# Kernel tuning notes

Measured on AMD Instinct MI355X. Metric: run time of the kernel, lower is better.

Reference implementation:

```python
import jax, jax.numpy as jnp
import numpy as np
from jax import lax

# PointPWC multi-scale Chamfer/Smoothness/Curvature loss (single scale here).
F_CHAMFER = 1.0
F_SMOOTH = 0.5
F_CURVATURE = 0.3
ALPHA0 = 0.02


def _sqdist(src, dst):
    # src: (B,N,3), dst: (B,M,3) -> (B,N,M) squared euclidean distances
    d = -2.0 * jnp.einsum('bnc,bmc->bnm', src, dst)
    d = d + jnp.sum(src * src, axis=-1)[:, :, None]
    d = d + jnp.sum(dst * dst, axis=-1)[:, None, :]
    return d


def _knn(sqd, k):
    # smallest-k of sqd along last axis -> (dists, indices)
    neg, idx = lax.top_k(-sqd, k)
    return -neg, idx


def _group(points, idx):
    # points: (B,N,C), idx: (B,M,k) -> (B,M,k,C)
    return jax.vmap(lambda p, i: p[i])(points, idx)


def _curvature(pc):
    # pc: (B,N,3) -> (B,N,3)
    _, kidx = _knn(_sqdist(pc, pc), 10)
    grouped = _group(pc, kidx)
    return jnp.sum(grouped - pc[:, :, None, :], axis=2) / 9.0


def _curvature_warp(pc, warped):
    _, kidx = _knn(_sqdist(pc, pc), 10)
    grouped = _group(warped, kidx)
    return jnp.sum(grouped - warped[:, :, None, :], axis=2) / 9.0


def _chamfer(p1, p2):
    sqd = _sqdist(p1, p2)
    return jnp.min(sqd, axis=-1), jnp.min(sqd, axis=1)


def _smooth(pc, flow, k):
    _, kidx = _knn(_sqdist(pc, pc), k)
    g = _group(flow, kidx)
    d = g - flow[:, :, None, :]
    sq = jnp.sum(d * d, axis=3)
    # safe norm: zero (self-neighbor) entries get norm 0 with zero grad
    nrm = jnp.where(sq == 0, 0.0, jnp.sqrt(jnp.where(sq == 0, 1.0, sq)))
    return jnp.sum(nrm, axis=2) / 8.0


def _interp_curvature(p1, p2, c2):
    dist, kidx = _knn(_sqdist(p1, p2), 5)
    g = _group(c2, kidx)  # (B,N,5,3)
    w = 1.0 / (dist + 1e-8)
    w = w / jnp.sum(w, axis=2, keepdims=True)
    return jnp.sum(w[..., None] * g, axis=2)


def setup_inputs() -> dict:
    key = jax.random.key(0)
    k1, k2, k3 = jax.random.split(key, 3)
    N = 8192
    coords = jax.random.normal(k1, (N, 3), dtype=jnp.float32)
    registration_gt = jax.random.normal(k2, (1, N, 3), dtype=jnp.float32)
    registration_pred = jax.random.normal(k3, (1, N, 3), dtype=jnp.float32)
    return {
        'registration_pred': registration_pred,
        'registration_gt': registration_gt,
        'coords': coords,
        'smoothness_k': 9,
    }


def reference(registration_pred, registration_gt, coords, smoothness_k):
    pc1 = coords[None]                       # (1,N,3)
    pc2 = coords[None] + registration_gt     # (1,N,3)
    flow = registration_pred                 # (1,N,3)

    pc2_curv = _curvature(pc2)
    pc1_warp = pc1 + flow
    dist1, dist2 = _chamfer(pc1_warp, pc2)
    moved_curv = _curvature_warp(pc1, pc1_warp)

    chamfer = jnp.mean(jnp.sum(dist1, axis=1)) + jnp.mean(jnp.sum(dist2, axis=1))
    smooth = jnp.mean(jnp.sum(_smooth(pc1, flow, smoothness_k), axis=1))
    inter_curv = _interp_curvature(pc1_warp, pc2, pc2_curv)
    curv = jnp.mean(jnp.sum(jnp.sum((inter_curv - moved_curv) ** 2, axis=2), axis=1))

    total = (F_CHAMFER * ALPHA0 * chamfer
             + F_CURVATURE * ALPHA0 * curv
             + F_SMOOTH * ALPHA0 * smooth)
    return jnp.reshape(total, (1,))
```

## Files before the change

kernel.cpp:

```cpp
#include <hip/hip_runtime.h>
#include <math.h>

#define N_PTS 8192
#define QPW 4
#define QPW_REV 8
#define WPB 4
#define QPB (QPW * WPB)
#define BLKS_TOPK (N_PTS / QPB)
#define BLKS_REV  (N_PTS / (QPW_REV * WPB))

#define R0_END BLKS_TOPK
#define R1_END (2 * BLKS_TOPK)
#define R3_END (3 * BLKS_TOPK)
#define GRID_TOTAL (3 * BLKS_TOPK + BLKS_REV)

#define W_CHAM 0.02f
#define W_CURV 0.006f
#define W_SMOO 0.01f

#define BIGF 1e30f
#define IDX_MASK 0x1FFFu
#define KEY_MASK 0xFFFFE000u

__device__ __forceinline__ float mkkey(float d, unsigned idx) {
    return __uint_as_float((__float_as_uint(d) & KEY_MASK) | idx);
}
__device__ __forceinline__ int keyidx(float k) {
    return (int)(__float_as_uint(k) & IDX_MASK);
}
__device__ __forceinline__ unsigned monou(float k) {
    int b = __float_as_int(k);
    return (unsigned)(b ^ ((b >> 31) | 0x80000000));
}
__device__ __forceinline__ int prefcnt(unsigned long long m) {
    return __builtin_amdgcn_mbcnt_hi((unsigned)(m >> 32),
           __builtin_amdgcn_mbcnt_lo((unsigned)m, 0));
}

template <int K>
__device__ __forceinline__ void kinsert(float kv, float (&bd)[K]) {
    bd[K - 1] = kv;
#pragma unroll
    for (int s = K - 1; s > 0; --s) {
        float lo = fminf(bd[s - 1], bd[s]);
        float hi = fmaxf(bd[s - 1], bd[s]);
        bd[s - 1] = lo; bd[s] = hi;
    }
}

template <int K>
__device__ void merge_keys(float m1, float m2, float m3, float (&bd)[K], int lane) {
    float h0 = m1, h1 = m2, h2 = m3;
#pragma unroll
    for (int r = 0; r < K; ++r) {
        float bv = h0;
#pragma unroll
        for (int off = 1; off < 64; off <<= 1) bv = fminf(bv, __shfl_xor(bv, off));
        bd[r] = bv;
        if (h0 == bv) { h0 = h1; h1 = h2; h2 = BIGF; }
    }
}

template <int K>
__device__ void tau_rescan(const float4* __restrict__ cand,
                           float nqx, float nqy, float nqz, float tau,
                           float (&bd)[K], int lane) {
#pragma unroll
    for (int r = 0; r < K; ++r) bd[r] = BIGF;
    const float4* cp = cand + lane;
    unsigned ib = (unsigned)lane;
    for (int it = 0; it < N_PTS / 64; ++it) {
        float4 p = cp[it * 64];
        float d = fmaf(p.x, nqx, fmaf(p.y, nqy, fmaf(p.z, nqz, p.w)));
        float kc = mkkey(d, ib);
        unsigned long long m = __ballot(kc <= tau);
        while (m) {
            int b = __builtin_ctzll(m);
            m &= m - 1;
            float kv = __shfl(kc, b);
            if (kv < bd[K - 1]) kinsert<K>(kv, bd);
        }
        ib += 64;
    }
}

template <int K>
__device__ void select_set(const float4* __restrict__ cand,
                           float nqx, float nqy, float nqz,
                           float& k1, float& k2, float& k3,
                           bool& q1, bool& q2, bool& q3, float& km, int lane) {
    const unsigned u1 = monou(k1), u2 = monou(k2), u3 = monou(k3);
    float bmn = k1, bmx = k1;
#pragma unroll
    for (int off = 1; off < 64; off <<= 1) {
        bmn = fminf(bmn, __shfl_xor(bmn, off));
        bmx = fmaxf(bmx, __shfl_xor(bmx, off));
    }
    unsigned lo = monou(bmn), hi = monou(bmx), piv = 0u;
    int cnt = -1;
    unsigned long long b3 = 0ull;
    for (int it = 0; it < 34; ++it) {
        piv = lo + ((hi - lo) >> 1);
        unsigned long long b1 = __ballot(u1 <= piv);
        unsigned long long b2 = __ballot(u2 <= piv);
        b3 = __ballot(u3 <= piv);
        cnt = __popcll(b1) + __popcll(b2) + __popcll(b3);
        if (cnt == K) break;
        if (cnt < K) lo = piv + 1; else hi = piv - 1;
    }
    bool setok = (cnt == K);
    bool fail;
    float bdK[K];
    if (setok) {
        q1 = (u1 <= piv); q2 = (u2 <= piv); q3 = (u3 <= piv);
        float t = q3 ? k3 : (q2 ? k2 : (q1 ? k1 : -BIGF));
#pragma unroll
        for (int off = 1; off < 64; off <<= 1) t = fmaxf(t, __shfl_xor(t, off));
        km = t;
        fail = (b3 != 0ull);
    } else {
        merge_keys<K>(k1, k2, k3, bdK, lane);
        km = bdK[K - 1];
        fail = (__ballot(k3 <= km) != 0ull);
    }
    if (fail) { tau_rescan<K>(cand, nqx, nqy, nqz, km, bdK, lane); setok = false; }
    if (!setok) {
        float kv = BIGF;
#pragma unroll
        for (int r = 0; r < K; ++r) if (lane == r) kv = bdK[r];
        k1 = kv; k2 = BIGF; k3 = BIGF;
        q1 = (lane < K); q2 = false; q3 = false;
        km = bdK[K - 1];
    }
}

__device__ __forceinline__ void wave_add3(float& a, float& b, float& c) {
#pragma unroll
    for (int off = 1; off < 64; off <<= 1) {
        a += __shfl_xor(a, off);
        b += __shfl_xor(b, off);
        c += __shfl_xor(c, off);
    }
}
__device__ __forceinline__ void wave_add4(float& a, float& b, float& c, float& d) {
#pragma unroll
    for (int off = 1; off < 64; off <<= 1) {
        a += __shfl_xor(a, off);
        b += __shfl_xor(b, off);
        c += __shfl_xor(c, off);
        d += __shfl_xor(d, off);
    }
}

template <int Q>
__device__ __forceinline__ void scank(const float4* __restrict__ cand,
                                      const float (&nqx)[Q], const float (&nqy)[Q],
                                      const float (&nqz)[Q],
                                      float (&m1)[Q], float (&m2)[Q], float (&m3)[Q],
                                      int lane) {
#pragma unroll
    for (int qi = 0; qi < Q; ++qi) { m1[qi] = BIGF; m2[qi] = BIGF; m3[qi] = BIGF; }
    const float4* cp = cand + lane;
    unsigned ib = (unsigned)lane;
#pragma unroll 2
    for (int it = 0; it < N_PTS / 256; ++it) {
        float4 p0 = cp[it * 256 + 0];
        float4 p1 = cp[it * 256 + 64];
        float4 p2 = cp[it * 256 + 128];
        float4 p3 = cp[it * 256 + 192];
#pragma unroll
        for (int qi = 0; qi < Q; ++qi) {
            float d0 = fmaf(p0.x, nqx[qi], fmaf(p0.y, nqy[qi], fmaf(p0.z, nqz[qi], p0.w)));
            float k0 = mkkey(d0, ib);
            m3[qi] = __builtin_amdgcn_fmed3f(k0, m2[qi], m3[qi]);
            m2[qi] = __builtin_amdgcn_fmed3f(k0, m1[qi], m2[qi]);
            m1[qi] = fminf(k0, m1[qi]);
            float d1 = fmaf(p1.x, nqx[qi], fmaf(p1.y, nqy[qi], fmaf(p1.z, nqz[qi], p1.w)));
            float k1 = mkkey(d1, ib + 64u);
            m3[qi] = __builtin_amdgcn_fmed3f(k1, m2[qi], m3[qi]);
            m2[qi] = __builtin_amdgcn_fmed3f(k1, m1[qi], m2[qi]);
            m1[qi] = fminf(k1, m1[qi]);
            float d2 = fmaf(p2.x, nqx[qi], fmaf(p2.y, nqy[qi], fmaf(p2.z, nqz[qi], p2.w)));
            float k2 = mkkey(d2, ib + 128u);
            m3[qi] = __builtin_amdgcn_fmed3f(k2, m2[qi], m3[qi]);
            m2[qi] = __builtin_amdgcn_fmed3f(k2, m1[qi], m2[qi]);
            m1[qi] = fminf(k2, m1[qi]);
            float d3 = fmaf(p3.x, nqx[qi], fmaf(p3.y, nqy[qi], fmaf(p3.z, nqz[qi], p3.w)));
            float k3 = mkkey(d3, ib + 192u);
            m3[qi] = __builtin_amdgcn_fmed3f(k3, m2[qi], m3[qi]);
            m2[qi] = __builtin_amdgcn_fmed3f(k3, m1[qi], m2[qi]);
            m1[qi] = fminf(k3, m1[qi]);
        }
        ib += 256u;
    }
}

__global__ void prep_kernel(const float* __restrict__ flow, const float* __restrict__ gt,
                            const float* __restrict__ coords,
                            float4* __restrict__ p1q, float4* __restrict__ p2q,
                            float4* __restrict__ wq, float* __restrict__ accs,
                            int* __restrict__ done) {
    int i = blockIdx.x * blockDim.x + threadIdx.x;
    if (i < N_PTS) {
        float cx = coords[3 * i + 0], cy = coords[3 * i + 1], cz = coords[3 * i + 2];
        float p2x = cx + gt[3 * i + 0], p2y = cy + gt[3 * i + 1], p2z = cz + gt[3 * i + 2];
        float wx = cx + flow[3 * i + 0], wy = cy + flow[3 * i + 1], wz = cz + flow[3 * i + 2];
        p1q[i] = make_float4(cx, cy, cz, cx * cx + cy * cy + cz * cz);
        p2q[i] = make_float4(p2x, p2y, p2z, p2x * p2x + p2y * p2y + p2z * p2z);
        wq[i]  = make_float4(wx, wy, wz, wx * wx + wy * wy + wz * wz);
    }
    if (i < 8) accs[i] = 0.0f;
    if (i == 8) done[0] = 0;
}

__global__ __launch_bounds__(256) void fused4_kernel(const float4* __restrict__ p1q,
                                                     const float4* __restrict__ p2q,
                                                     const float4* __restrict__ wq,
                                                     const float* __restrict__ flow,
                                                     const int* __restrict__ ksm_p,
                                                     float* __restrict__ curv2,
                                                     float* __restrict__ mcurv,
                                                     float* __restrict__ crossk,
                                                     float* __restrict__ accs) {
    const int tid = threadIdx.x, lane = tid & 63, wv = tid >> 6;
    const int b = blockIdx.x;

    if (b >= R3_END) {
        __shared__ float pmn[WPB];
        const int q0 = (b - R3_END) * (QPW_REV * WPB) + wv * QPW_REV;
        float nqx[QPW_REV], nqy[QPW_REV], nqz[QPW_REV], qw[QPW_REV], mn[QPW_REV];
#pragma unroll
        for (int qi = 0; qi < QPW_REV; ++qi) {
            float4 t = p2q[q0 + qi];
            nqx[qi] = -2.f * t.x; nqy[qi] = -2.f * t.y; nqz[qi] = -2.f * t.z;
            qw[qi] = t.w; mn[qi] = BIGF;
        }
        const float4* cp = wq + lane;
#pragma unroll 2
        for (int it = 0; it < N_PTS / 128; ++it) {
            float4 p0 = cp[it * 128 + 0];
            float4 p1 = cp[it * 128 + 64];
#pragma unroll
            for (int qi = 0; qi < QPW_REV; ++qi) {
                float d0 = fmaf(p0.x, nqx[qi], fmaf(p0.y, nqy[qi], fmaf(p0.z, nqz[qi], p0.w)));
                float d1 = fmaf(p1.x, nqx[qi], fmaf(p1.y, nqy[qi], fmaf(p1.z, nqz[qi], p1.w)));
                mn[qi] = fminf(mn[qi], fminf(d0, d1));
            }
        }
        float s = 0.f;
#pragma unroll
        for (int qi = 0; qi < QPW_REV; ++qi) {
            float v = mn[qi];
#pragma unroll
            for (int off = 1; off < 64; off <<= 1) v = fminf(v, __shfl_xor(v, off));
            s += v + qw[qi];
        }
        if (lane == 0) pmn[wv] = s;
        __syncthreads();
        if (tid == 0) atomicAdd(&accs[1], pmn[0] + pmn[1] + pmn[2] + pmn[3]);
        return;
    }

    const int role = (b < R0_END) ? 0 : (b < R1_END) ? 1 : 3;
    const int blk = b - ((role == 0) ? 0 : (role == 1) ? R0_END : R1_END);
    const int q0 = blk * QPB + wv * QPW;

    const float4* qsrc = (role == 0) ? p2q : (role == 1) ? p1q : wq;
    const float4* cand = (role == 1) ? p1q : p2q;
    float nqx[QPW], nqy[QPW], nqz[QPW];
#pragma unroll
    for (int qi = 0; qi < QPW; ++qi) {
        float4 t = qsrc[q0 + qi];
        nqx[qi] = -2.f * t.x; nqy[qi] = -2.f * t.y; nqz[qi] = -2.f * t.z;
    }
    float m1[QPW], m2[QPW], m3[QPW];
    scank<QPW>(cand, nqx, nqy, nqz, m1, m2, m3, lane);

    if (role == 3) {
        constexpr int K = 5;
#pragma unroll
        for (int qi = 0; qi < QPW; ++qi) {
            float k1 = m1[qi], k2 = m2[qi], k3 = m3[qi]; bool q1, q2, q3; float km;
            select_set<K>(p2q, nqx[qi], nqy[qi], nqz[qi], k1, k2, k3, q1, q2, q3, km, lane);
            const int q = q0 + qi;
            unsigned long long b1 = __ballot(q1), b2 = __ballot(q2), b3 = __ballot(q3);
            int c1 = __popcll(b1), c2 = __popcll(b2);
            if (q1) crossk[prefcnt(b1) * N_PTS + q] = k1;
            if (q2) crossk[(c1 + prefcnt(b2)) * N_PTS + q] = k2;
            if (q3) crossk[(c1 + c2 + prefcnt(b3)) * N_PTS + q] = k3;
        }
        return;
    }

    constexpr int K = 10;
    if (role == 0) {
#pragma unroll
        for (int qi = 0; qi < QPW; ++qi) {
            float k1 = m1[qi], k2 = m2[qi], k3 = m3[qi]; bool q1, q2, q3; float km;
            select_set<K>(p2q, nqx[qi], nqy[qi], nqz[qi], k1, k2, k3, q1, q2, q3, km, lane);
            float ax = 0.f, ay = 0.f, az = 0.f;
            if (q1) { float4 nb = p2q[keyidx(k1)]; ax += nb.x; ay += nb.y; az += nb.z; }
            if (q2) { float4 nb = p2q[keyidx(k2)]; ax += nb.x; ay += nb.y; az += nb.z; }
            if (q3) { float4 nb = p2q[keyidx(k3)]; ax += nb.x; ay += nb.y; az += nb.z; }
            wave_add3(ax, ay, az);
            if (lane == 0) {
                const int q = q0 + qi;
                float4 t = p2q[q];
                curv2[q * 3 + 0] = (ax - 10.f * t.x) * (1.f / 9.f);
                curv2[q * 3 + 1] = (ay - 10.f * t.y) * (1.f / 9.f);
                curv2[q * 3 + 2] = (az - 10.f * t.z) * (1.f / 9.f);
            }
        }
    } else {
        __shared__ float psm[WPB];
        const bool iall = (ksm_p[0] >= 10);
        float smsum = 0.f;
#pragma unroll
        for (int qi = 0; qi < QPW; ++qi) {
            float k1 = m1[qi], k2 = m2[qi], k3 = m3[qi]; bool q1, q2, q3; float km;
            select_set<K>(p1q, nqx[qi], nqy[qi], nqz[qi], k1, k2, k3, q1, q2, q3, km, lane);
            const int q = q0 + qi;
            const float fqx = flow[q * 3 + 0], fqy = flow[q * 3 + 1], fqz = flow[q * 3 + 2];
            float ax = 0.f, ay = 0.f, az = 0.f, sm = 0.f;
            if (q1) {
                const int ni = keyidx(k1);
                float4 nb = wq[ni];
                ax += nb.x; ay += nb.y; az += nb.z;
                if (iall || k1 < km) {
                    float dx = flow[ni * 3 + 0] - fqx, dy = flow[ni * 3 + 1] - fqy, dz = flow[ni * 3 + 2] - fqz;
                    float sq = dx * dx + dy * dy + dz * dz;
                    sm += (sq == 0.f) ? 0.f : sqrtf(sq);
                }
            }
            if (q2) {
                const int ni = keyidx(k2);
                float4 nb = wq[ni];
                ax += nb.x; ay += nb.y; az += nb.z;
                if (iall || k2 < km) {
                    float dx = flow[ni * 3 + 0] - fqx, dy = flow[ni * 3 + 1] - fqy, dz = flow[ni * 3 + 2] - fqz;
                    float sq = dx * dx + dy * dy + dz * dz;
                    sm += (sq == 0.f) ? 0.f : sqrtf(sq);
                }
            }
            if (q3) {
                const int ni = keyidx(k3);
                float4 nb = wq[ni];
                ax += nb.x; ay += nb.y; az += nb.z;
                if (iall || k3 < km) {
                    float dx = flow[ni * 3 + 0] - fqx, dy = flow[ni * 3 + 1] - fqy, dz = flow[ni * 3 + 2] - fqz;
                    float sq = dx * dx + dy * dy + dz * dz;
                    sm += (sq == 0.f) ? 0.f : sqrtf(sq);
                }
            }
            wave_add4(ax, ay, az, sm);
            smsum += sm * 0.125f;
            if (lane == 0) {
                float4 wqp = wq[q];
                mcurv[q * 3 + 0] = (ax - 10.f * wqp.x) * (1.f / 9.f);
                mcurv[q * 3 + 1] = (ay - 10.f * wqp.y) * (1.f / 9.f);
                mcurv[q * 3 + 2] = (az - 10.f * wqp.z) * (1.f / 9.f);
            }
        }
        if (lane == 0) psm[wv] = smsum;
        __syncthreads();
        if (tid == 0) atomicAdd(&accs[2], psm[0] + psm[1] + psm[2] + psm[3]);
    }
}

__global__ __launch_bounds__(64) void epi_kernel(const float* __restrict__ crossk,
                                                 const float4* __restrict__ wq,
                                                 const float4* __restrict__ p2q,
                                                 const float* __restrict__ curv2,
                                                 const float* __restrict__ mcurv,
                                                 float* __restrict__ accs,
                                                 int* __restrict__ done,
                                                 float* __restrict__ out) {
    const int lane = threadIdx.x & 63;
    const int q = blockIdx.x * 64 + threadIdx.x;
    constexpr int K = 5;
    float4 qp = wq[q];
    float bd[K]; int bi[K];
#pragma unroll
    for (int r = 0; r < K; ++r) {
        bi[r] = keyidx(crossk[r * N_PTS + q]);
        float4 nb = p2q[bi[r]];
        float dx = qp.x - nb.x, dy = qp.y - nb.y, dz = qp.z - nb.z;
        bd[r] = dx * dx + dy * dy + dz * dz;
    }
    float w[K], wsum = 0.f;
#pragma unroll
    for (int r = 0; r < K; ++r) { w[r] = 1.f / (bd[r] + 1e-8f); wsum += w[r]; }
    float ix = 0.f, iy = 0.f, iz = 0.f;
#pragma unroll
    for (int r = 0; r < K; ++r) {
        float ww = w[r] / wsum;
        ix += ww * curv2[bi[r] * 3 + 0];
        iy += ww * curv2[bi[r] * 3 + 1];
        iz += ww * curv2[bi[r] * 3 + 2];
    }
    float dx = ix - mcurv[q * 3 + 0];
    float dy = iy - mcurv[q * 3 + 1];
    float dz = iz - mcurv[q * 3 + 2];
    float d1 = fminf(fminf(fminf(bd[0], bd[1]), fminf(bd[2], bd[3])), bd[4]);
    float cv = dx * dx + dy * dy + dz * dz;
#pragma unroll
    for (int off = 1; off < 64; off <<= 1) {
        d1 += __shfl_xor(d1, off);
        cv += __shfl_xor(cv, off);
    }
    if (lane == 0) {
        atomicAdd(&accs[0], d1);
        atomicAdd(&accs[3], cv);
        __threadfence();
        int v = atomicAdd(done, 1);
        if (v == (int)gridDim.x - 1) {
            out[0] = W_CHAM * (accs[0] + accs[1]) + W_CURV * accs[3] + W_SMOO * accs[2];
        }
    }
}

extern "C" void kernel_launch(void* const* d_in, const int* in_sizes, int n_in,
                              void* d_out, int out_size, void* d_ws, size_t ws_size,
                              hipStream_t stream) {
    const float* flow   = (const float*)d_in[0];
    const float* gt     = (const float*)d_in[1];
    const float* coords = (const float*)d_in[2];
    const int*   ksm    = (const int*)d_in[3];

    float4* p1q   = (float4*)d_ws;
    float4* p2q   = p1q + N_PTS;
    float4* wq    = p2q + N_PTS;
    float*  curv2 = (float*)(wq + N_PTS);
    float*  mcurv = curv2 + 3 * N_PTS;
    float*  crossk = mcurv + 3 * N_PTS;
    float*  accs  = crossk + 5 * N_PTS;
    int*    done  = (int*)(accs + 8);
    float*  out   = (float*)d_out;

    prep_kernel<<<(N_PTS + 255) / 256, 256, 0, stream>>>(flow, gt, coords, p1q, p2q, wq,
                                                         accs, done);
    fused4_kernel<<<GRID_TOTAL, 256, 0, stream>>>(p1q, p2q, wq, flow, ksm,
                                                  curv2, mcurv, crossk, accs);
    epi_kernel<<<N_PTS / 64, 64, 0, stream>>>(crossk, wq, p2q, curv2, mcurv,
                                              accs, done, out);
}
```

Measured before the change: 144.9 us.

## Stage candidate points through double-buffered LDS tiles in brute-force scans

The candidate scans in both the top-k and reverse-chamfer paths now cooperatively load 512-point strips into a double-buffered shared-memory tile instead of each wave reading candidates straight from global memory. The four waves in a block share each strip, which cuts redundant global/L2 traffic. In exchange it adds a block-wide barrier per strip and 16 KB of LDS per block, which can lower occupancy. The per-point math is unchanged.

```diff
diff --git a/kernel.cpp b/kernel.cpp
--- a/kernel.cpp
+++ b/kernel.cpp
@@ -13,6 +13,9 @@
 #define R1_END (2 * BLKS_TOPK)
 #define R3_END (3 * BLKS_TOPK)
 #define GRID_TOTAL (3 * BLKS_TOPK + BLKS_REV)
+
+#define STRIP 512
+#define NSTRIP (N_PTS / STRIP)
 
 #define W_CHAM 0.02f
 #define W_CURV 0.006f
@@ -153,45 +156,57 @@
 }
 
 template <int Q>
-__device__ __forceinline__ void scank(const float4* __restrict__ cand,
-                                      const float (&nqx)[Q], const float (&nqy)[Q],
-                                      const float (&nqz)[Q],
-                                      float (&m1)[Q], float (&m2)[Q], float (&m3)[Q],
-                                      int lane) {
+__device__ __forceinline__ void scank_lds(const float4* __restrict__ cand,
+                                          float4 (&tile)[2][STRIP],
+                                          const float (&nqx)[Q], const float (&nqy)[Q],
+                                          const float (&nqz)[Q],
+                                          float (&m1)[Q], float (&m2)[Q], float (&m3)[Q],
+                                          int tid, int lane) {
 #pragma unroll
     for (int qi = 0; qi < Q; ++qi) { m1[qi] = BIGF; m2[qi] = BIGF; m3[qi] = BIGF; }
-    const float4* cp = cand + lane;
-    unsigned ib = (unsigned)lane;
-#pragma unroll 2
-    for (int it = 0; it < N_PTS / 256; ++it) {
-        float4 p0 = cp[it * 256 + 0];
-        float4 p1 = cp[it * 256 + 64];
-        float4 p2 = cp[it * 256 + 128];
-        float4 p3 = cp[it * 256 + 192];
-#pragma unroll
-        for (int qi = 0; qi < Q; ++qi) {
-            float d0 = fmaf(p0.x, nqx[qi], fmaf(p0.y, nqy[qi], fmaf(p0.z, nqz[qi], p0.w)));
-            float k0 = mkkey(d0, ib);
-            m3[qi] = __builtin_amdgcn_fmed3f(k0, m2[qi], m3[qi]);
-            m2[qi] = __builtin_amdgcn_fmed3f(k0, m1[qi], m2[qi]);
-            m1[qi] = fminf(k0, m1[qi]);
-            float d1 = fmaf(p1.x, nqx[qi], fmaf(p1.y, nqy[qi], fmaf(p1.z, nqz[qi], p1.w)));
-            float k1 = mkkey(d1, ib + 64u);
-            m3[qi] = __builtin_amdgcn_fmed3f(k1, m2[qi], m3[qi]);
-            m2[qi] = __builtin_amdgcn_fmed3f(k1, m1[qi], m2[qi]);
-            m1[qi] = fminf(k1, m1[qi]);
-            float d2 = fmaf(p2.x, nqx[qi], fmaf(p2.y, nqy[qi], fmaf(p2.z, nqz[qi], p2.w)));
-            float k2 = mkkey(d2, ib + 128u);
-            m3[qi] = __builtin_amdgcn_fmed3f(k2, m2[qi], m3[qi]);
-            m2[qi] = __builtin_amdgcn_fmed3f(k2, m1[qi], m2[qi]);
-            m1[qi] = fminf(k2, m1[qi]);
-            float d3 = fmaf(p3.x, nqx[qi], fmaf(p3.y, nqy[qi], fmaf(p3.z, nqz[qi], p3.w)));
-            float k3 = mkkey(d3, ib + 192u);
-            m3[qi] = __builtin_amdgcn_fmed3f(k3, m2[qi], m3[qi]);
-            m2[qi] = __builtin_amdgcn_fmed3f(k3, m1[qi], m2[qi]);
-            m1[qi] = fminf(k3, m1[qi]);
-        }
-        ib += 256u;
+    tile[0][tid] = cand[tid];
+    tile[0][tid + 256] = cand[tid + 256];
+    __syncthreads();
+    for (int s = 0; s < NSTRIP; ++s) {
+        const int cur = s & 1, nb = cur ^ 1;
+        if (s + 1 < NSTRIP) {
+            tile[nb][tid] = cand[(s + 1) * STRIP + tid];
+            tile[nb][tid + 256] = cand[(s + 1) * STRIP + tid + 256];
+        }
+        const float4* tp = tile[cur];
+        unsigned ib = (unsigned)(s * STRIP + lane);
+#pragma unroll
+        for (int j = 0; j < STRIP / 256; ++j) {
+            float4 p0 = tp[j * 256 + lane];
+            float4 p1 = tp[j * 256 + 64 + lane];
+            float4 p2 = tp[j * 256 + 128 + lane];
+            float4 p3 = tp[j * 256 + 192 + lane];
+#pragma unroll
+            for (int qi = 0; qi < Q; ++qi) {
+                float d0 = fmaf(p0.x, nqx[qi], fmaf(p0.y, nqy[qi], fmaf(p0.z, nqz[qi], p0.w)));
+                float k0 = mkkey(d0, ib);
+                m3[qi] = __builtin_amdgcn_fmed3f(k0, m2[qi], m3[qi]);
+                m2[qi] = __builtin_amdgcn_fmed3f(k0, m1[qi], m2[qi]);
+                m1[qi] = fminf(k0, m1[qi]);
+                float d1 = fmaf(p1.x, nqx[qi], fmaf(p1.y, nqy[qi], fmaf(p1.z, nqz[qi], p1.w)));
+                float k1 = mkkey(d1, ib + 64u);
+                m3[qi] = __builtin_amdgcn_fmed3f(k1, m2[qi], m3[qi]);
+                m2[qi] = __builtin_amdgcn_fmed3f(k1, m1[qi], m2[qi]);
+                m1[qi] = fminf(k1, m1[qi]);
+                float d2 = fmaf(p2.x, nqx[qi], fmaf(p2.y, nqy[qi], fmaf(p2.z, nqz[qi], p2.w)));
+                float k2 = mkkey(d2, ib + 128u);
+                m3[qi] = __builtin_amdgcn_fmed3f(k2, m2[qi], m3[qi]);
+                m2[qi] = __builtin_amdgcn_fmed3f(k2, m1[qi], m2[qi]);
+                m1[qi] = fminf(k2, m1[qi]);
+                float d3 = fmaf(p3.x, nqx[qi], fmaf(p3.y, nqy[qi], fmaf(p3.z, nqz[qi], p3.w)));
+                float k3 = mkkey(d3, ib + 192u);
+                m3[qi] = __builtin_amdgcn_fmed3f(k3, m2[qi], m3[qi]);
+                m2[qi] = __builtin_amdgcn_fmed3f(k3, m1[qi], m2[qi]);
+                m1[qi] = fminf(k3, m1[qi]);
+            }
+            ib += 256u;
+        }
+        __syncthreads();
     }
 }
 
@@ -224,6 +239,7 @@
                                                      float* __restrict__ accs) {
     const int tid = threadIdx.x, lane = tid & 63, wv = tid >> 6;
     const int b = blockIdx.x;
+    __shared__ float4 tile[2][STRIP];
 
     if (b >= R3_END) {
         __shared__ float pmn[WPB];
@@ -235,17 +251,28 @@
             nqx[qi] = -2.f * t.x; nqy[qi] = -2.f * t.y; nqz[qi] = -2.f * t.z;
             qw[qi] = t.w; mn[qi] = BIGF;
         }
-        const float4* cp = wq + lane;
-#pragma unroll 2
-        for (int it = 0; it < N_PTS / 128; ++it) {
-            float4 p0 = cp[it * 128 + 0];
-            float4 p1 = cp[it * 128 + 64];
-#pragma unroll
-            for (int qi = 0; qi < QPW_REV; ++qi) {
-                float d0 = fmaf(p0.x, nqx[qi], fmaf(p0.y, nqy[qi], fmaf(p0.z, nqz[qi], p0.w)));
-                float d1 = fmaf(p1.x, nqx[qi], fmaf(p1.y, nqy[qi], fmaf(p1.z, nqz[qi], p1.w)));
-                mn[qi] = fminf(mn[qi], fminf(d0, d1));
-            }
+        tile[0][tid] = wq[tid];
+        tile[0][tid + 256] = wq[tid + 256];
+        __syncthreads();
+        for (int s = 0; s < NSTRIP; ++s) {
+            const int cur = s & 1, nb = cur ^ 1;
+            if (s + 1 < NSTRIP) {
+                tile[nb][tid] = wq[(s + 1) * STRIP + tid];
+                tile[nb][tid + 256] = wq[(s + 1) * STRIP + tid + 256];
+            }
+            const float4* tp = tile[cur];
+#pragma unroll
+            for (int j = 0; j < STRIP / 128; ++j) {
+                float4 p0 = tp[j * 128 + lane];
+                float4 p1 = tp[j * 128 + 64 + lane];
+#pragma unroll
+                for (int qi = 0; qi < QPW_REV; ++qi) {
+                    float d0 = fmaf(p0.x, nqx[qi], fmaf(p0.y, nqy[qi], fmaf(p0.z, nqz[qi], p0.w)));
+                    float d1 = fmaf(p1.x, nqx[qi], fmaf(p1.y, nqy[qi], fmaf(p1.z, nqz[qi], p1.w)));
+                    mn[qi] = fminf(mn[qi], fminf(d0, d1));
+                }
+            }
+            __syncthreads();
         }
         float s = 0.f;
 #pragma unroll
@@ -274,7 +301,7 @@
         nqx[qi] = -2.f * t.x; nqy[qi] = -2.f * t.y; nqz[qi] = -2.f * t.z;
     }
     float m1[QPW], m2[QPW], m3[QPW];
-    scank<QPW>(cand, nqx, nqy, nqz, m1, m2, m3, lane);
+    scank_lds<QPW>(cand, tile, nqx, nqy, nqz, m1, m2, m3, tid, lane);
 
     if (role == 3) {
         constexpr int K = 5;
```

After: 143.9 us. About the same (-0.7%).
